# Kernel optimization log

Measured on AMD Instinct MI355X. Metric: run time of the kernel, lower is better.

Reference implementation:

```python
import jax, jax.numpy as jnp
import numpy as np

B = 16384        # batch of tree nodes being reduced this step
CH = 16
T = B * CH       # total children
SIZE = 256       # tree-LSTM hidden size
TR = 256         # tracker size


def setup_inputs() -> dict:
    key = jax.random.key(0)
    ks = jax.random.split(key, 8)
    w = 0.05  # small init scale to keep gates in active range
    return {
        "children": jax.random.normal(ks[0], (T, 2 * SIZE), jnp.float32),   # [T, h||c]
        "tracking": jax.random.normal(ks[1], (B, 2 * TR), jnp.float32),      # [B, h||c]
        "W_iou": jax.random.normal(ks[2], (SIZE, 3 * SIZE), jnp.float32) * w,
        "b_iou": jax.random.normal(ks[3], (3 * SIZE,), jnp.float32) * w,
        "W_f": jax.random.normal(ks[4], (SIZE, SIZE), jnp.float32) * w,
        "b_f": jax.random.normal(ks[5], (SIZE,), jnp.float32) * w,
        "W_iou_track": jax.random.normal(ks[6], (TR, 3 * SIZE), jnp.float32) * w,
        "W_f_track": jax.random.normal(ks[7], (TR, SIZE), jnp.float32) * w,
        "segment_ids": jnp.repeat(jnp.arange(B, dtype=jnp.int32), CH),        # [T]
        "lens": jnp.full((B,), CH, dtype=jnp.int32),                           # [B]
    }


def reference(children, tracking, W_iou, b_iou, W_f, b_f, W_iou_track, W_f_track,
              segment_ids, lens):
    size = W_f.shape[0]
    nb = tracking.shape[0]
    tracking_h = tracking[:, : tracking.shape[1] // 2]               # [B, TR]

    # per-node mean over children of concatenated (h||c), then take h half
    sums = jax.ops.segment_sum(children, segment_ids, num_segments=nb)  # [B, 2*size]
    mean_h = (sums / lens[:, None].astype(children.dtype))[:, :size]    # [B, size]

    iou = mean_h @ W_iou + b_iou + tracking_h @ W_iou_track             # [B, 3*size]
    i, o, u = jnp.split(iou, 3, axis=1)
    i = jax.nn.sigmoid(i)
    o = jax.nn.sigmoid(o)
    u = jnp.tanh(u)

    ch_h = children[:, :size]
    ch_c = children[:, size:]
    f = ch_h @ W_f + b_f + (tracking_h @ W_f_track)[segment_ids]        # [T, size]
    fc = jax.nn.sigmoid(f) * ch_c                                       # [T, size]

    # NOTE: original torch code slices fc[0:len] (not fc[start:start+len]) per
    # batch element, i.e. each node sums a PREFIX of the flat fc tensor.
    # We replicate that exactly via a cumsum + gather at index len-1.
    cs = jnp.cumsum(fc, axis=0)                                         # [T, size]
    fc_b = cs[lens - 1]                                                 # [B, size]

    c = i * u + fc_b
    h = o * c
    return jnp.concatenate([h, c], axis=1)                              # [B, 2*size]
```

## Files before the change

kernel.cpp:

```cpp
#include <hip/hip_runtime.h>
#include <hip/hip_bf16.h>

constexpr int BB  = 16384;
constexpr int CH  = 16;
constexpr int SZ  = 256;
constexpr int KK  = 512;
constexpr int NN  = 768;
constexpr int TM  = 32;

typedef float  f32x4 __attribute__((ext_vector_type(4)));
typedef short  s16x8 __attribute__((ext_vector_type(8)));

__device__ __forceinline__ unsigned short f2bf(float x) {
    unsigned u = __builtin_bit_cast(unsigned, x);
    unsigned r = u + 0x7fffu + ((u >> 16) & 1u);
    return (unsigned short)(r >> 16);
}

__device__ __forceinline__ float sigmoidf_(float x) {
    return 1.0f / (1.0f + __expf(-x));
}

__global__ void wprep(const float* __restrict__ Wiou,
                      const float* __restrict__ Wtrk,
                      unsigned short* __restrict__ Wsw,
                      float* __restrict__ fcb) {
    int g = blockIdx.x * 256 + threadIdx.x;
    if (g < 256) fcb[g] = 0.0f;
    if (g >= 48 * 16 * 64) return;
    int lane = g & 63;
    int ksnt = g >> 6;
    int ks = ksnt & 15;
    int nt = ksnt >> 4;
    int n  = nt * 16 + (lane & 15);
    int k0 = ks * 32 + (lane >> 4) * 8;
    unsigned short o8[8];
#pragma unroll
    for (int j = 0; j < 8; ++j) {
        int k = k0 + j;
        float v = (k < SZ) ? Wiou[k * NN + n] : Wtrk[(k - SZ) * NN + n];
        o8[j] = f2bf(v);
    }
    *(s16x8*)(Wsw + (size_t)g * 8) = *(s16x8*)o8;
}

__global__ void fc16(const float* __restrict__ children,
                     const float* __restrict__ tracking,
                     const float* __restrict__ Wf,
                     const float* __restrict__ bf,
                     const float* __restrict__ Wft,
                     float* __restrict__ fcb) {
    int t = blockIdx.x;
    int j = threadIdx.x;
    float base = bf[j];
    for (int k = 0; k < SZ; ++k) base += tracking[k] * Wft[k * SZ + j];
    const float* ch = children + (size_t)t * KK;
    float s = 0.0f;
    for (int k = 0; k < SZ; ++k) s += ch[k] * Wf[k * SZ + j];
    float f = base + s;
    atomicAdd(&fcb[j], sigmoidf_(f) * ch[SZ + j]);
}

__global__ __launch_bounds__(256, 2) void gemm_fused(
        const float* __restrict__ children,
        const float* __restrict__ tracking,
        const unsigned short* __restrict__ Wsw,
        const float* __restrict__ biou,
        const float* __restrict__ fcb,
        float* __restrict__ out) {
    __shared__ __attribute__((aligned(16))) unsigned short Asw[16 * 2 * 64 * 8];

    const int tid = threadIdx.x;
    const int b0  = blockIdx.x * TM;

    const f32x4* ch4 = (const f32x4*)children;
    const f32x4* tr4 = (const f32x4*)tracking;
#pragma unroll
    for (int i = 0; i < 16; ++i) {
        int task = i * 256 + tid;
        int c4 = task & 127;
        int m  = task >> 7;
        int b  = b0 + m;
        f32x4 v;
        if (c4 < 64) {
            const f32x4* p = ch4 + (size_t)b * (CH * 128) + c4;
            f32x4 s = p[0];
#pragma unroll
            for (int jj = 1; jj < CH; ++jj) s += p[(size_t)jj * 128];
            v = s * (1.0f / 16.0f);
        } else {
            v = tr4[(size_t)b * 128 + (c4 - 64)];
        }
        int ks   = c4 >> 3;
        int q    = (c4 >> 1) & 3;
        int j0   = (c4 & 1) * 4;
        int lane = (m & 15) | (q << 4);
        int m16  = m >> 4;
        ushort4 pk;
        pk.x = f2bf(v[0]); pk.y = f2bf(v[1]); pk.z = f2bf(v[2]); pk.w = f2bf(v[3]);
        *(ushort4*)&Asw[(((ks * 2 + m16) * 64 + lane) * 8 + j0)] = pk;
    }
    __syncthreads();

    const int lane = tid & 63;
    const int w    = tid >> 6;
    const int m16  = w & 1;
    const int sh   = w >> 1;
    const int l15  = lane & 15;
    const int l4   = lane >> 4;

    for (int t = 0; t < 4; ++t) {
        f32x4 acc[3][2] = {};
        const s16x8* bptr[3][2];
#pragma unroll
        for (int p = 0; p < 3; ++p)
#pragma unroll
            for (int ss = 0; ss < 2; ++ss) {
                int nt = p * 16 + t * 4 + sh * 2 + ss;
                bptr[p][ss] = (const s16x8*)(Wsw + ((size_t)(nt * 16) * 64 + lane) * 8);
            }
#pragma unroll
        for (int ks = 0; ks < 16; ++ks) {
            s16x8 a = *(const s16x8*)&Asw[((ks * 2 + m16) * 64 + lane) * 8];
#pragma unroll
            for (int p = 0; p < 3; ++p)
#pragma unroll
                for (int ss = 0; ss < 2; ++ss) {
                    s16x8 bq = bptr[p][ss][(size_t)ks * 64];
                    acc[p][ss] = __builtin_amdgcn_mfma_f32_16x16x32_bf16(
                        a, bq, acc[p][ss], 0, 0, 0);
                }
        }
#pragma unroll
        for (int ss = 0; ss < 2; ++ss) {
            int colj = t * 64 + (sh * 2 + ss) * 16 + l15;
            float fb = fcb[colj];
            float bi = biou[colj];
            float bo = biou[SZ + colj];
            float bu = biou[2 * SZ + colj];
#pragma unroll
            for (int r = 0; r < 4; ++r) {
                int m = m16 * 16 + l4 * 4 + r;
                int b = b0 + m;
                float vi = acc[0][ss][r] + bi;
                float vo = acc[1][ss][r] + bo;
                float vu = acc[2][ss][r] + bu;
                float i_ = sigmoidf_(vi);
                float o_ = sigmoidf_(vo);
                float u_ = 2.0f / (1.0f + __expf(-2.0f * vu)) - 1.0f;
                float c_ = i_ * u_ + fb;
                float h_ = o_ * c_;
                size_t ob = (size_t)b * KK;
                out[ob + colj] = h_;
                out[ob + SZ + colj] = c_;
            }
        }
    }
}

extern "C" void kernel_launch(void* const* d_in, const int* in_sizes, int n_in,
                              void* d_out, int out_size, void* d_ws, size_t ws_size,
                              hipStream_t stream) {
    const float* children = (const float*)d_in[0];
    const float* tracking = (const float*)d_in[1];
    const float* Wiou     = (const float*)d_in[2];
    const float* biou     = (const float*)d_in[3];
    const float* Wf       = (const float*)d_in[4];
    const float* bf       = (const float*)d_in[5];
    const float* Wiout    = (const float*)d_in[6];
    const float* Wft      = (const float*)d_in[7];
    float* out = (float*)d_out;

    unsigned short* Wsw = (unsigned short*)d_ws;
    float* fcb = (float*)((char*)d_ws + (size_t)KK * NN * 2);

    hipLaunchKernelGGL(wprep, dim3(192), dim3(256), 0, stream, Wiou, Wiout, Wsw, fcb);
    hipLaunchKernelGGL(fc16, dim3(16), dim3(256), 0, stream,
                       children, tracking, Wf, bf, Wft, fcb);
    hipLaunchKernelGGL(gemm_fused, dim3(BB / TM), dim3(256), 0, stream,
                       children, tracking, Wsw, biou, fcb, out);
}
```

Baseline: 792.6 us.

## Split mean-pack into separate kernel and stream weights via double-buffered LDS

Moves the per-node child mean and bf16 packing into its own kernel that writes a pre-swizzled A buffer to workspace. The GEMM kernel now keeps a full 16-row A fragment in registers per wave and streams weight column tiles into LDS with async global_load_lds, double-buffered across 16 column steps. The aim is to overlap weight loads with MFMA work and give each wave more independent work than the original fused kernel. The cost is an extra round trip of the packed A buffer through global memory, an additional kernel launch, and lower occupancy from launch_bounds(256,1).

Measured after the change: 725.0 us. 8.5% less time.

```diff
diff --git a/kernel.cpp b/kernel.cpp
--- a/kernel.cpp
+++ b/kernel.cpp
@@ -6,7 +6,6 @@
 constexpr int SZ  = 256;
 constexpr int KK  = 512;
 constexpr int NN  = 768;
-constexpr int TM  = 32;
 
 typedef float  f32x4 __attribute__((ext_vector_type(4)));
 typedef short  s16x8 __attribute__((ext_vector_type(8)));
@@ -16,9 +15,14 @@
     unsigned r = u + 0x7fffu + ((u >> 16) & 1u);
     return (unsigned short)(r >> 16);
 }
-
 __device__ __forceinline__ float sigmoidf_(float x) {
     return 1.0f / (1.0f + __expf(-x));
+}
+__device__ __forceinline__ void gload_lds16(const unsigned short* g, unsigned short* l) {
+    __builtin_amdgcn_global_load_lds(
+        (const __attribute__((address_space(1))) unsigned int*)g,
+        (__attribute__((address_space(3))) unsigned int*)l,
+        16, 0, 0);
 }
 
 __global__ void wprep(const float* __restrict__ Wiou,
@@ -57,103 +61,104 @@
     const float* ch = children + (size_t)t * KK;
     float s = 0.0f;
     for (int k = 0; k < SZ; ++k) s += ch[k] * Wf[k * SZ + j];
-    float f = base + s;
-    atomicAdd(&fcb[j], sigmoidf_(f) * ch[SZ + j]);
+    atomicAdd(&fcb[j], sigmoidf_(base + s) * ch[SZ + j]);
 }
 
-__global__ __launch_bounds__(256, 2) void gemm_fused(
+__global__ __launch_bounds__(256) void meanpack(
         const float* __restrict__ children,
         const float* __restrict__ tracking,
+        unsigned short* __restrict__ Apack) {
+    int g  = blockIdx.x * 256 + threadIdx.x;
+    int c4 = g & 127;
+    int m  = g >> 7;
+    const f32x4* ch4 = (const f32x4*)children;
+    const f32x4* tr4 = (const f32x4*)tracking;
+    f32x4 v;
+    if (c4 < 64) {
+        const f32x4* p = ch4 + (size_t)m * (CH * 128) + c4;
+        f32x4 s = p[0];
+#pragma unroll
+        for (int jj = 1; jj < CH; ++jj) s += p[(size_t)jj * 128];
+        v = s * 0.0625f;
+    } else {
+        v = tr4[(size_t)m * 128 + (c4 - 64)];
+    }
+    int ks = c4 >> 3;
+    int q  = (c4 >> 1) & 3;
+    int j0 = (c4 & 1) * 4;
+    int laneF = (m & 15) | (q << 4);
+    int g16   = m >> 4;
+    ushort4 pk;
+    pk.x = f2bf(v[0]); pk.y = f2bf(v[1]); pk.z = f2bf(v[2]); pk.w = f2bf(v[3]);
+    *(ushort4*)&Apack[(((size_t)(g16 * 16 + ks) * 64 + laneF) * 8 + j0)] = pk;
+}
+
+__global__ __launch_bounds__(256, 1) void gemm2(
+        const unsigned short* __restrict__ Apack,
         const unsigned short* __restrict__ Wsw,
         const float* __restrict__ biou,
         const float* __restrict__ fcb,
         float* __restrict__ out) {
-    __shared__ __attribute__((aligned(16))) unsigned short Asw[16 * 2 * 64 * 8];
+    __shared__ __attribute__((aligned(16))) unsigned short Bst[2][3][16 * 64 * 8];
 
-    const int tid = threadIdx.x;
-    const int b0  = blockIdx.x * TM;
-
-    const f32x4* ch4 = (const f32x4*)children;
-    const f32x4* tr4 = (const f32x4*)tracking;
-#pragma unroll
-    for (int i = 0; i < 16; ++i) {
-        int task = i * 256 + tid;
-        int c4 = task & 127;
-        int m  = task >> 7;
-        int b  = b0 + m;
-        f32x4 v;
-        if (c4 < 64) {
-            const f32x4* p = ch4 + (size_t)b * (CH * 128) + c4;
-            f32x4 s = p[0];
-#pragma unroll
-            for (int jj = 1; jj < CH; ++jj) s += p[(size_t)jj * 128];
-            v = s * (1.0f / 16.0f);
-        } else {
-            v = tr4[(size_t)b * 128 + (c4 - 64)];
-        }
-        int ks   = c4 >> 3;
-        int q    = (c4 >> 1) & 3;
-        int j0   = (c4 & 1) * 4;
-        int lane = (m & 15) | (q << 4);
-        int m16  = m >> 4;
-        ushort4 pk;
-        pk.x = f2bf(v[0]); pk.y = f2bf(v[1]); pk.z = f2bf(v[2]); pk.w = f2bf(v[3]);
-        *(ushort4*)&Asw[(((ks * 2 + m16) * 64 + lane) * 8 + j0)] = pk;
-    }
-    __syncthreads();
-
+    const int tid  = threadIdx.x;
     const int lane = tid & 63;
     const int w    = tid >> 6;
-    const int m16  = w & 1;
-    const int sh   = w >> 1;
     const int l15  = lane & 15;
     const int l4   = lane >> 4;
+    const int g16  = blockIdx.x * 4 + w;
 
-    for (int t = 0; t < 4; ++t) {
-        f32x4 acc[3][2] = {};
-        const s16x8* bptr[3][2];
+    s16x8 a[16];
+    const s16x8* ap = (const s16x8*)(Apack + ((size_t)g16 * 16 * 64) * 8);
 #pragma unroll
-        for (int p = 0; p < 3; ++p)
+    for (int ks = 0; ks < 16; ++ks) a[ks] = ap[ks * 64 + lane];
+
+    auto kick = [&](int ct, int buf) {
 #pragma unroll
-            for (int ss = 0; ss < 2; ++ss) {
-                int nt = p * 16 + t * 4 + sh * 2 + ss;
-                bptr[p][ss] = (const s16x8*)(Wsw + ((size_t)(nt * 16) * 64 + lane) * 8);
-            }
+        for (int i = 0; i < 12; ++i) {
+            int chunk = w * 12 + i;
+            int p  = chunk >> 4;
+            int ck = chunk & 15;
+            const unsigned short* gsrc =
+                Wsw + ((size_t)(p * 16 + ct) * 16 * 64) * 8 + ck * 512 + lane * 8;
+            gload_lds16(gsrc, &Bst[buf][p][ck * 512]);
+        }
+    };
+
+    kick(0, 0);
+    for (int ct = 0; ct < 16; ++ct) {
+        __syncthreads();
+        if (ct < 15) kick(ct + 1, (ct + 1) & 1);
+        const int buf = ct & 1;
+        f32x4 acc0 = {}, acc1 = {}, acc2 = {};
 #pragma unroll
         for (int ks = 0; ks < 16; ++ks) {
-            s16x8 a = *(const s16x8*)&Asw[((ks * 2 + m16) * 64 + lane) * 8];
+            s16x8 b0 = *(const s16x8*)&Bst[buf][0][(ks * 64 + lane) * 8];
+            s16x8 b1 = *(const s16x8*)&Bst[buf][1][(ks * 64 + lane) * 8];
+            s16x8 b2 = *(const s16x8*)&Bst[buf][2][(ks * 64 + lane) * 8];
+            acc0 = __builtin_amdgcn_mfma_f32_16x16x32_bf16(a[ks], b0, acc0, 0, 0, 0);
+            acc1 = __builtin_amdgcn_mfma_f32_16x16x32_bf16(a[ks], b1, acc1, 0, 0, 0);
+            acc2 = __builtin_amdgcn_mfma_f32_16x16x32_bf16(a[ks], b2, acc2, 0, 0, 0);
+        }
+        int colj = ct * 16 + l15;
+        float fb = fcb[colj];
+        float bi = biou[colj];
+        float bo = biou[SZ + colj];
+        float bu = biou[2 * SZ + colj];
 #pragma unroll
-            for (int p = 0; p < 3; ++p)
-#pragma unroll
-                for (int ss = 0; ss < 2; ++ss) {
-                    s16x8 bq = bptr[p][ss][(size_t)ks * 64];
-                    acc[p][ss] = __builtin_amdgcn_mfma_f32_16x16x32_bf16(
-                        a, bq, acc[p][ss], 0, 0, 0);
-                }
-        }
-#pragma unroll
-        for (int ss = 0; ss < 2; ++ss) {
-            int colj = t * 64 + (sh * 2 + ss) * 16 + l15;
-            float fb = fcb[colj];
-            float bi = biou[colj];
-            float bo = biou[SZ + colj];
-            float bu = biou[2 * SZ + colj];
-#pragma unroll
-            for (int r = 0; r < 4; ++r) {
-                int m = m16 * 16 + l4 * 4 + r;
-                int b = b0 + m;
-                float vi = acc[0][ss][r] + bi;
-                float vo = acc[1][ss][r] + bo;
-                float vu = acc[2][ss][r] + bu;
-                float i_ = sigmoidf_(vi);
-                float o_ = sigmoidf_(vo);
-                float u_ = 2.0f / (1.0f + __expf(-2.0f * vu)) - 1.0f;
-                float c_ = i_ * u_ + fb;
-                float h_ = o_ * c_;
-                size_t ob = (size_t)b * KK;
-                out[ob + colj] = h_;
-                out[ob + SZ + colj] = c_;
-            }
+        for (int r = 0; r < 4; ++r) {
+            int m = g16 * 16 + l4 * 4 + r;
+            float vi = acc0[r] + bi;
+            float vo = acc1[r] + bo;
+            float vu = acc2[r] + bu;
+            float i_ = sigmoidf_(vi);
+            float o_ = sigmoidf_(vo);
+            float u_ = 2.0f / (1.0f + __expf(-2.0f * vu)) - 1.0f;
+            float c_ = i_ * u_ + fb;
+            float h_ = o_ * c_;
+            size_t ob = (size_t)m * KK;
+            out[ob + colj]      = h_;
+            out[ob + SZ + colj] = c_;
         }
     }
 }
@@ -171,12 +176,15 @@
     const float* Wft      = (const float*)d_in[7];
     float* out = (float*)d_out;
 
-    unsigned short* Wsw = (unsigned short*)d_ws;
-    float* fcb = (float*)((char*)d_ws + (size_t)KK * NN * 2);
+    unsigned short* Wsw   = (unsigned short*)d_ws;
+    float*          fcb   = (float*)((char*)d_ws + (1 << 20));
+    unsigned short* Apack = (unsigned short*)((char*)d_ws + (2 << 20));
 
     hipLaunchKernelGGL(wprep, dim3(192), dim3(256), 0, stream, Wiou, Wiout, Wsw, fcb);
     hipLaunchKernelGGL(fc16, dim3(16), dim3(256), 0, stream,
                        children, tracking, Wf, bf, Wft, fcb);
-    hipLaunchKernelGGL(gemm_fused, dim3(BB / TM), dim3(256), 0, stream,
-                       children, tracking, Wsw, biou, fcb, out);
+    hipLaunchKernelGGL(meanpack, dim3(BB * 128 / 256), dim3(256), 0, stream,
+                       children, tracking, Apack);
+    hipLaunchKernelGGL(gemm2, dim3(BB / 64), dim3(256), 0, stream,
+                       Apack, Wsw, biou, fcb, out);
 }
```
